# Performance work log

Hardware: AMD Instinct MI355X
Metric: run time of the kernel (lower is better)

Reference implementation:

```python
import jax, jax.numpy as jnp
import numpy as np

B, X, Y, Z = 8, 32, 32, 32
Dx = Dy = Dz = 128
K = 256   # h_dim * k, k=1
H = 2     # h_out
EPS = 1e-5


def _wn(V, g):
    # weight_norm with dim=None: W = g * V / ||V||_F (g scalar)
    return (g / jnp.linalg.norm(V)) * V


def setup_inputs() -> dict:
    key = jax.random.key(0)
    ks = jax.random.split(key, 8)
    x = jax.random.normal(ks[0], (B, X, Dx), jnp.float32)
    y = jax.random.normal(ks[1], (B, Y, Dy), jnp.float32)
    z = jax.random.normal(ks[2], (B, Z, Dz), jnp.float32)
    Vx = jax.random.normal(ks[3], (K, Dx), jnp.float32) * 0.05
    Vy = jax.random.normal(ks[4], (K, Dy), jnp.float32) * 0.05
    Vz = jax.random.normal(ks[5], (K, Dz), jnp.float32) * 0.05
    Vh = jax.random.normal(ks[6], (H, K), jnp.float32) * 0.05
    return {
        "x": x, "y": y, "z": z,
        "Vx": Vx, "gx": jnp.linalg.norm(Vx), "bx": jnp.zeros((K,), jnp.float32),
        "Vy": Vy, "gy": jnp.linalg.norm(Vy), "by": jnp.zeros((K,), jnp.float32),
        "Vz": Vz, "gz": jnp.linalg.norm(Vz), "bz": jnp.zeros((K,), jnp.float32),
        "Vh": Vh, "gh": jnp.linalg.norm(Vh), "bh": jnp.zeros((H,), jnp.float32),
        "gamma": jnp.ones((K,), jnp.float32), "beta": jnp.zeros((K,), jnp.float32),
    }


def reference(x, y, z, Vx, gx, bx, Vy, gy, by, Vz, gz, bz, Vh, gh, bh, gamma, beta):
    relu = jax.nn.relu
    _x = relu(x @ _wn(Vx, gx).T + bx)  # [B,X,K]
    _y = relu(y @ _wn(Vy, gy).T + by)  # [B,Y,K]
    _z = relu(z @ _wn(Vz, gz).T + bz)  # [B,Z,K]
    # trilinear outer product: [B,X,Y,Z,K] (memory-explosive intermediate)
    xyz = jnp.einsum('bxk,byk,bzk->bxyzk', _x, _y, _z)
    att = jnp.einsum('bxyzk,hk->bhxyz', xyz, _wn(Vh, gh)) + bh[None, :, None, None, None]
    # softmax over flattened X*Y*Z per head
    att = jax.nn.softmax(att.reshape(B, H, -1), axis=-1).reshape(B, H, X, Y, Z)
    # attention pooling, summed over all h_out heads (equals the torch loop)
    att_sum = att.sum(axis=1)  # [B,X,Y,Z]
    logits = jnp.einsum('bxk,byk,bzk,bxyz->bk', _x, _y, _z, att_sum)  # [B,K]
    # BatchNorm1d (training-mode batch stats, biased variance)
    mean = logits.mean(axis=0)
    var = logits.var(axis=0)
    out = (logits - mean) / jnp.sqrt(var + EPS) * gamma + beta
    return (out, att)
```

## Files before the change

### kernel.cpp

```cpp
#include <hip/hip_runtime.h>
#include <math.h>

#define BB 8
#define XD 32
#define DD 128
#define KK 256
#define HH 2
#define XYZ 32768
#define EPSV 1e-5f

#define WS_X    0
#define WS_Y    65536
#define WS_Z    131072
#define WS_RAW  196608
#define WS_PART (WS_RAW + 524288)

__global__ void __launch_bounds__(256)
tan_proj_kernel(const float* x, const float* y, const float* z,
                const float* Vx, const float* Vy, const float* Vz,
                const float* gx, const float* gy, const float* gz,
                const float* bx, const float* by, const float* bz,
                float* ws) {
    __shared__ float lin[4 * DD];
    __shared__ float wred[4];
    int bid = blockIdx.x;
    int which = bid >> 6;
    int rgrp = bid & 63;
    int r0 = rgrp * 4;
    const float *in, *V, *g, *bias;
    float* outp;
    if (which == 0)      { in = x; V = Vx; g = gx; bias = bx; outp = ws + WS_X; }
    else if (which == 1) { in = y; V = Vy; g = gy; bias = by; outp = ws + WS_Y; }
    else                 { in = z; V = Vz; g = gz; bias = bz; outp = ws + WS_Z; }
    int t = threadIdx.x;
    {
        int f0 = t, f1 = t + 256;
        lin[f0] = in[(r0 + (f0 >> 7)) * DD + (f0 & 127)];
        lin[f1] = in[(r0 + (f1 >> 7)) * DD + (f1 & 127)];
    }
    __syncthreads();
    const float4* v4 = (const float4*)(V + t * DD);
    const float4* l4 = (const float4*)lin;
    float a0 = 0.f, a1 = 0.f, a2 = 0.f, a3 = 0.f, ssp = 0.f;
#pragma unroll 8
    for (int d4 = 0; d4 < DD / 4; ++d4) {
        float4 a = v4[d4];
        ssp += a.x * a.x + a.y * a.y + a.z * a.z + a.w * a.w;
        float4 b0 = l4[d4];
        float4 b1 = l4[32 + d4];
        float4 b2 = l4[64 + d4];
        float4 b3 = l4[96 + d4];
        a0 += a.x * b0.x + a.y * b0.y + a.z * b0.z + a.w * b0.w;
        a1 += a.x * b1.x + a.y * b1.y + a.z * b1.z + a.w * b1.w;
        a2 += a.x * b2.x + a.y * b2.y + a.z * b2.z + a.w * b2.w;
        a3 += a.x * b3.x + a.y * b3.y + a.z * b3.z + a.w * b3.w;
    }
#pragma unroll
    for (int o = 32; o > 0; o >>= 1) ssp += __shfl_xor(ssp, o);
    if ((t & 63) == 0) wred[t >> 6] = ssp;
    __syncthreads();
    float ss = wred[0] + wred[1] + wred[2] + wred[3];
    float scale = g[0] * rsqrtf(ss);
    float bv = bias[t];
    outp[(r0 + 0) * KK + t] = fmaxf(a0 * scale + bv, 0.f);
    outp[(r0 + 1) * KK + t] = fmaxf(a1 * scale + bv, 0.f);
    outp[(r0 + 2) * KK + t] = fmaxf(a2 * scale + bv, 0.f);
    outp[(r0 + 3) * KK + t] = fmaxf(a3 * scale + bv, 0.f);
}

__global__ void __launch_bounds__(256)
tan_score_kernel(const float* Vh, const float* gh, const float* bh, float* ws) {
    __shared__ float ys[32 * 256];
    __shared__ float zs[32 * 256];
    __shared__ float shh;
    int t = threadIdx.x;
    int bb = blockIdx.x >> 5;
    int xx = blockIdx.x & 31;
    const float* _xb = ws + WS_X + (bb * 32 + xx) * KK;
    const float* _yb = ws + WS_Y + bb * 8192;
    const float* _zb = ws + WS_Z + bb * 8192;

    if (t < 64) {
        float4 h1 = *(const float4*)(Vh + t * 8);
        float4 h2 = *(const float4*)(Vh + t * 8 + 4);
        float hs = h1.x * h1.x + h1.y * h1.y + h1.z * h1.z + h1.w * h1.w
                 + h2.x * h2.x + h2.y * h2.y + h2.z * h2.z + h2.w * h2.w;
#pragma unroll
        for (int o = 32; o > 0; o >>= 1) hs += __shfl_xor(hs, o);
        if (t == 0) shh = hs;
    }

#pragma unroll
    for (int i = 0; i < 8; ++i) {
        int flat = i * 1024 + t * 4;
        int row = flat >> 8;
        int k = flat & 255;
        int gsw = (((k >> 2) ^ (row & 7)) << 2);
        *(float4*)(ys + row * 256 + gsw) = *(const float4*)(_yb + flat);
        *(float4*)(zs + row * 256 + gsw) = *(const float4*)(_zb + flat);
    }
    __syncthreads();
    float sh = gh[0] * rsqrtf(shh);

    int ty = t >> 4;
    int tz = t & 15;
    int y0 = ty, y1 = ty + 16;
    int z0 = tz, z1 = tz + 16;
    int ysw0 = (y0 & 7), ysw1 = (y1 & 7);
    int zsw0 = (z0 & 7), zsw1 = (z1 & 7);

    float a000 = 0.f, a001 = 0.f, a010 = 0.f, a011 = 0.f;
    float a100 = 0.f, a101 = 0.f, a110 = 0.f, a111 = 0.f;

#pragma unroll 4
    for (int kc = 0; kc < 256; kc += 4) {
        int g = kc >> 2;
        float4 xv  = *(const float4*)(_xb + kc);
        float4 vh0 = *(const float4*)(Vh + kc);
        float4 vh1 = *(const float4*)(Vh + KK + kc);
        float4 ya = *(const float4*)(ys + y0 * 256 + ((g ^ ysw0) << 2));
        float4 yb = *(const float4*)(ys + y1 * 256 + ((g ^ ysw1) << 2));
        float4 za = *(const float4*)(zs + z0 * 256 + ((g ^ zsw0) << 2));
        float4 zb = *(const float4*)(zs + z1 * 256 + ((g ^ zsw1) << 2));
#define TAN_STEP(c) { \
        float xs = sh * xv.c; \
        float w0 = xs * vh0.c, w1 = xs * vh1.c; \
        float t00 = w0 * ya.c, t01 = w0 * yb.c; \
        float t10 = w1 * ya.c, t11 = w1 * yb.c; \
        a000 = fmaf(t00, za.c, a000); a001 = fmaf(t00, zb.c, a001); \
        a010 = fmaf(t01, za.c, a010); a011 = fmaf(t01, zb.c, a011); \
        a100 = fmaf(t10, za.c, a100); a101 = fmaf(t10, zb.c, a101); \
        a110 = fmaf(t11, za.c, a110); a111 = fmaf(t11, zb.c, a111); }
        TAN_STEP(x) TAN_STEP(y) TAN_STEP(z) TAN_STEP(w)
#undef TAN_STEP
    }

    float b0 = bh[0], b1 = bh[1];
    float* r0 = ws + WS_RAW + (bb * 2 + 0) * XYZ + xx * 1024;
    float* r1 = r0 + XYZ;
    r0[y0 * 32 + z0] = a000 + b0;  r0[y0 * 32 + z1] = a001 + b0;
    r0[y1 * 32 + z0] = a010 + b0;  r0[y1 * 32 + z1] = a011 + b0;
    r1[y0 * 32 + z0] = a100 + b1;  r1[y0 * 32 + z1] = a101 + b1;
    r1[y1 * 32 + z0] = a110 + b1;  r1[y1 * 32 + z1] = a111 + b1;
}

__global__ void __launch_bounds__(1024)
tan_softmax_kernel(float* ws, float* out) {
    __shared__ float red[1024];
    int bh = blockIdx.x;
    int t = threadIdx.x;
    const float4* raw4 = (const float4*)(ws + WS_RAW + bh * XYZ);
    float4* att4 = (float4*)(out + BB * KK + bh * XYZ);
    float4 v[8];
#pragma unroll
    for (int i = 0; i < 8; ++i) v[i] = raw4[i * 1024 + t];
    float m = -1e30f;
#pragma unroll
    for (int i = 0; i < 8; ++i)
        m = fmaxf(m, fmaxf(fmaxf(v[i].x, v[i].y), fmaxf(v[i].z, v[i].w)));
    red[t] = m;
    __syncthreads();
    for (int s = 512; s > 0; s >>= 1) {
        if (t < s) red[t] = fmaxf(red[t], red[t + s]);
        __syncthreads();
    }
    float M = red[0];
    __syncthreads();
    float l = 0.f;
#pragma unroll
    for (int i = 0; i < 8; ++i) {
        v[i].x = __expf(v[i].x - M); v[i].y = __expf(v[i].y - M);
        v[i].z = __expf(v[i].z - M); v[i].w = __expf(v[i].w - M);
        l += v[i].x + v[i].y + v[i].z + v[i].w;
    }
    red[t] = l;
    __syncthreads();
    for (int s = 512; s > 0; s >>= 1) {
        if (t < s) red[t] += red[t + s];
        __syncthreads();
    }
    float inv = 1.f / red[0];
#pragma unroll
    for (int i = 0; i < 8; ++i) {
        float4 o = v[i];
        o.x *= inv; o.y *= inv; o.z *= inv; o.w *= inv;
        att4[i * 1024 + t] = o;
    }
}

__global__ void __launch_bounds__(256)
tan_logits_kernel(float* ws, const float* out) {
    __shared__ float as4[1024];
    int b = blockIdx.x >> 5;
    int x = blockIdx.x & 31;
    int t = threadIdx.x;
    const float* _zb = ws + WS_Z + b * 8192;
    float zreg[32];
#pragma unroll
    for (int zi = 0; zi < 32; ++zi) zreg[zi] = _zb[zi * 256 + t];
    const float* a0 = out + BB * KK + (b * 2) * XYZ + x * 1024;
    const float* a1 = a0 + XYZ;
    for (int i = t; i < 1024; i += 256) as4[i] = a0[i] + a1[i];
    __syncthreads();
    const float* _yb = ws + WS_Y + b * 8192;
    float acc = 0.f;
#pragma unroll 4
    for (int y = 0; y < 32; ++y) {
        float s = 0.f;
        const float4* ar = (const float4*)(as4 + y * 32);
#pragma unroll
        for (int j = 0; j < 8; ++j) {
            float4 a = ar[j];
            s += a.x * zreg[j * 4] + a.y * zreg[j * 4 + 1]
               + a.z * zreg[j * 4 + 2] + a.w * zreg[j * 4 + 3];
        }
        acc = fmaf(_yb[y * 256 + t], s, acc);
    }
    float xv = ws[WS_X + (b * 32 + x) * 256 + t];
    ws[WS_PART + (b * 32 + x) * 256 + t] = xv * acc;
}

__global__ void __launch_bounds__(1024)
tan_bn_kernel(float* ws, const float* gamma, const float* beta, float* out) {
    __shared__ float red[8192];
    int t = threadIdx.x;
    int tg = t >> 8;
    int k = t & 255;
    const float* part = ws + WS_PART;
    float lg[BB];
#pragma unroll
    for (int b = 0; b < BB; ++b) {
        float s = 0.f;
#pragma unroll
        for (int xi = 0; xi < 8; ++xi)
            s += part[(b * 32 + tg * 8 + xi) * 256 + k];
        red[tg * 2048 + b * 256 + k] = s;
    }
    __syncthreads();
    if (tg == 0) {
#pragma unroll
        for (int b = 0; b < BB; ++b)
            lg[b] = red[b * 256 + k] + red[2048 + b * 256 + k]
                  + red[4096 + b * 256 + k] + red[6144 + b * 256 + k];
        float mean = 0.f;
#pragma unroll
        for (int b = 0; b < BB; ++b) mean += lg[b];
        mean *= 0.125f;
        float var = 0.f;
#pragma unroll
        for (int b = 0; b < BB; ++b) { float d = lg[b] - mean; var += d * d; }
        var *= 0.125f;
        float inv = rsqrtf(var + EPSV);
        float gm = gamma[k], bt = beta[k];
#pragma unroll
        for (int b = 0; b < BB; ++b)
            out[b * 256 + k] = (lg[b] - mean) * inv * gm + bt;
    }
}

extern "C" void kernel_launch(void* const* d_in, const int* in_sizes, int n_in,
                              void* d_out, int out_size, void* d_ws, size_t ws_size,
                              hipStream_t stream) {
    (void)in_sizes; (void)n_in; (void)out_size; (void)ws_size;
    const float* x     = (const float*)d_in[0];
    const float* y     = (const float*)d_in[1];
    const float* z     = (const float*)d_in[2];
    const float* Vx    = (const float*)d_in[3];
    const float* gx    = (const float*)d_in[4];
    const float* bx    = (const float*)d_in[5];
    const float* Vy    = (const float*)d_in[6];
    const float* gy    = (const float*)d_in[7];
    const float* by    = (const float*)d_in[8];
    const float* Vz    = (const float*)d_in[9];
    const float* gz    = (const float*)d_in[10];
    const float* bz    = (const float*)d_in[11];
    const float* Vh    = (const float*)d_in[12];
    const float* gh    = (const float*)d_in[13];
    const float* bh    = (const float*)d_in[14];
    const float* gamma = (const float*)d_in[15];
    const float* beta  = (const float*)d_in[16];
    float* ws  = (float*)d_ws;
    float* out = (float*)d_out;

    tan_proj_kernel<<<192, 256, 0, stream>>>(x, y, z, Vx, Vy, Vz,
                                             gx, gy, gz, bx, by, bz, ws);
    tan_score_kernel<<<256, 256, 0, stream>>>(Vh, gh, bh, ws);
    tan_softmax_kernel<<<16, 1024, 0, stream>>>(ws, out);
    tan_logits_kernel<<<256, 256, 0, stream>>>(ws, out);
    tan_bn_kernel<<<1, 1024, 0, stream>>>(ws, gamma, beta, out);
}
```

Measured before the change: 129.2 us.

## Fuse softmax into score and logits kernels via online partial max/sum

Removes the standalone softmax kernel. The score kernel now computes per-block partial (max, sum-exp) statistics with an online-softmax warp reduction. The logits kernel merges the 32 partials per (batch, head), normalizes the raw scores, writes the attention output and builds the summed attention tile in one pass. The per-x partial logits are now accumulated with atomicAdd into a zeroed buffer, which simplifies the BN kernel, at the cost of an extra memset launch and nondeterministic float summation order.

```diff
diff --git a/kernel.cpp b/kernel.cpp
--- a/kernel.cpp
+++ b/kernel.cpp
@@ -13,7 +13,8 @@
 #define WS_Y    65536
 #define WS_Z    131072
 #define WS_RAW  196608
-#define WS_PART (WS_RAW + 524288)
+#define WS_SM   (WS_RAW + 524288)
+#define WS_LOG  (WS_SM + 1024)
 
 __global__ void __launch_bounds__(256)
 tan_proj_kernel(const float* x, const float* y, const float* z,
@@ -73,6 +74,7 @@
     __shared__ float ys[32 * 256];
     __shared__ float zs[32 * 256];
     __shared__ float shh;
+    __shared__ float smred[4][4];
     int t = threadIdx.x;
     int bb = blockIdx.x >> 5;
     int xx = blockIdx.x & 31;
@@ -105,7 +107,7 @@
     int ty = t >> 4;
     int tz = t & 15;
     int y0 = ty, y1 = ty + 16;
-    int z0 = tz, z1 = tz + 16;
+    int z0 = tz, z1 = tz + 15 + 1;
     int ysw0 = (y0 & 7), ysw1 = (y1 & 7);
     int zsw0 = (z0 & 7), zsw1 = (z1 & 7);
 
@@ -136,61 +138,57 @@
     }
 
     float b0 = bh[0], b1 = bh[1];
+    a000 += b0; a001 += b0; a010 += b0; a011 += b0;
+    a100 += b1; a101 += b1; a110 += b1; a111 += b1;
     float* r0 = ws + WS_RAW + (bb * 2 + 0) * XYZ + xx * 1024;
     float* r1 = r0 + XYZ;
-    r0[y0 * 32 + z0] = a000 + b0;  r0[y0 * 32 + z1] = a001 + b0;
-    r0[y1 * 32 + z0] = a010 + b0;  r0[y1 * 32 + z1] = a011 + b0;
-    r1[y0 * 32 + z0] = a100 + b1;  r1[y0 * 32 + z1] = a101 + b1;
-    r1[y1 * 32 + z0] = a110 + b1;  r1[y1 * 32 + z1] = a111 + b1;
-}
-
-__global__ void __launch_bounds__(1024)
-tan_softmax_kernel(float* ws, float* out) {
-    __shared__ float red[1024];
-    int bh = blockIdx.x;
-    int t = threadIdx.x;
-    const float4* raw4 = (const float4*)(ws + WS_RAW + bh * XYZ);
-    float4* att4 = (float4*)(out + BB * KK + bh * XYZ);
-    float4 v[8];
-#pragma unroll
-    for (int i = 0; i < 8; ++i) v[i] = raw4[i * 1024 + t];
-    float m = -1e30f;
-#pragma unroll
-    for (int i = 0; i < 8; ++i)
-        m = fmaxf(m, fmaxf(fmaxf(v[i].x, v[i].y), fmaxf(v[i].z, v[i].w)));
-    red[t] = m;
-    __syncthreads();
-    for (int s = 512; s > 0; s >>= 1) {
-        if (t < s) red[t] = fmaxf(red[t], red[t + s]);
-        __syncthreads();
-    }
-    float M = red[0];
-    __syncthreads();
-    float l = 0.f;
-#pragma unroll
-    for (int i = 0; i < 8; ++i) {
-        v[i].x = __expf(v[i].x - M); v[i].y = __expf(v[i].y - M);
-        v[i].z = __expf(v[i].z - M); v[i].w = __expf(v[i].w - M);
-        l += v[i].x + v[i].y + v[i].z + v[i].w;
-    }
-    red[t] = l;
-    __syncthreads();
-    for (int s = 512; s > 0; s >>= 1) {
-        if (t < s) red[t] += red[t + s];
-        __syncthreads();
-    }
-    float inv = 1.f / red[0];
-#pragma unroll
-    for (int i = 0; i < 8; ++i) {
-        float4 o = v[i];
-        o.x *= inv; o.y *= inv; o.z *= inv; o.w *= inv;
-        att4[i * 1024 + t] = o;
+    r0[y0 * 32 + z0] = a000;  r0[y0 * 32 + z1] = a001;
+    r0[y1 * 32 + z0] = a010;  r0[y1 * 32 + z1] = a011;
+    r1[y0 * 32 + z0] = a100;  r1[y0 * 32 + z1] = a101;
+    r1[y1 * 32 + z0] = a110;  r1[y1 * 32 + z1] = a111;
+
+    float m0 = fmaxf(fmaxf(a000, a001), fmaxf(a010, a011));
+    float l0 = __expf(a000 - m0) + __expf(a001 - m0)
+             + __expf(a010 - m0) + __expf(a011 - m0);
+    float m1 = fmaxf(fmaxf(a100, a101), fmaxf(a110, a111));
+    float l1 = __expf(a100 - m1) + __expf(a101 - m1)
+             + __expf(a110 - m1) + __expf(a111 - m1);
+#pragma unroll
+    for (int o = 1; o < 64; o <<= 1) {
+        float mo = __shfl_xor(m0, o), lo = __shfl_xor(l0, o);
+        float nm = fmaxf(m0, mo);
+        l0 = l0 * __expf(m0 - nm) + lo * __expf(mo - nm); m0 = nm;
+        mo = __shfl_xor(m1, o); lo = __shfl_xor(l1, o);
+        nm = fmaxf(m1, mo);
+        l1 = l1 * __expf(m1 - nm) + lo * __expf(mo - nm); m1 = nm;
+    }
+    if ((t & 63) == 0) {
+        int w = t >> 6;
+        smred[w][0] = m0; smred[w][1] = l0;
+        smred[w][2] = m1; smred[w][3] = l1;
+    }
+    __syncthreads();
+    if (t == 0) {
+        float M0 = smred[0][0], L0 = smred[0][1];
+        float M1 = smred[0][2], L1 = smred[0][3];
+#pragma unroll
+        for (int w = 1; w < 4; ++w) {
+            float nm = fmaxf(M0, smred[w][0]);
+            L0 = L0 * __expf(M0 - nm) + smred[w][1] * __expf(smred[w][0] - nm);
+            M0 = nm;
+            nm = fmaxf(M1, smred[w][2]);
+            L1 = L1 * __expf(M1 - nm) + smred[w][3] * __expf(smred[w][2] - nm);
+            M1 = nm;
+        }
+        float* sm = ws + WS_SM + (bb * 32 + xx) * 4;
+        sm[0] = M0; sm[1] = L0; sm[2] = M1; sm[3] = L1;
     }
 }
 
 __global__ void __launch_bounds__(256)
-tan_logits_kernel(float* ws, const float* out) {
+tan_logits_kernel(float* ws, float* out) {
     __shared__ float as4[1024];
+    __shared__ float cons[4];
     int b = blockIdx.x >> 5;
     int x = blockIdx.x & 31;
     int t = threadIdx.x;
@@ -198,10 +196,40 @@
     float zreg[32];
 #pragma unroll
     for (int zi = 0; zi < 32; ++zi) zreg[zi] = _zb[zi * 256 + t];
-    const float* a0 = out + BB * KK + (b * 2) * XYZ + x * 1024;
-    const float* a1 = a0 + XYZ;
-    for (int i = t; i < 1024; i += 256) as4[i] = a0[i] + a1[i];
-    __syncthreads();
+
+    if (t < 64) {
+        const float* sm = ws + WS_SM + (b * 32 + (t & 31)) * 4;
+        float4 p = *(const float4*)sm;
+        float m0 = p.x, l0 = p.y, m1 = p.z, l1 = p.w;
+#pragma unroll
+        for (int o = 1; o < 32; o <<= 1) {
+            float mo = __shfl_xor(m0, o), lo = __shfl_xor(l0, o);
+            float nm = fmaxf(m0, mo);
+            l0 = l0 * __expf(m0 - nm) + lo * __expf(mo - nm); m0 = nm;
+            mo = __shfl_xor(m1, o); lo = __shfl_xor(l1, o);
+            nm = fmaxf(m1, mo);
+            l1 = l1 * __expf(m1 - nm) + lo * __expf(mo - nm); m1 = nm;
+        }
+        if (t == 0) {
+            cons[0] = m0; cons[1] = 1.f / l0;
+            cons[2] = m1; cons[3] = 1.f / l1;
+        }
+    }
+    __syncthreads();
+    float M0 = cons[0], inv0 = cons[1], M1 = cons[2], inv1 = cons[3];
+    const float* r0 = ws + WS_RAW + (b * 2) * XYZ + x * 1024;
+    const float* r1 = r0 + XYZ;
+    float* o0 = out + BB * KK + (b * 2) * XYZ + x * 1024;
+    float* o1 = o0 + XYZ;
+#pragma unroll
+    for (int i = t; i < 1024; i += 256) {
+        float a0 = __expf(r0[i] - M0) * inv0;
+        float a1 = __expf(r1[i] - M1) * inv1;
+        o0[i] = a0; o1[i] = a1;
+        as4[i] = a0 + a1;
+    }
+    __syncthreads();
+
     const float* _yb = ws + WS_Y + b * 8192;
     float acc = 0.f;
 #pragma unroll 4
@@ -217,45 +245,29 @@
         acc = fmaf(_yb[y * 256 + t], s, acc);
     }
     float xv = ws[WS_X + (b * 32 + x) * 256 + t];
-    ws[WS_PART + (b * 32 + x) * 256 + t] = xv * acc;
-}
-
-__global__ void __launch_bounds__(1024)
-tan_bn_kernel(float* ws, const float* gamma, const float* beta, float* out) {
-    __shared__ float red[8192];
-    int t = threadIdx.x;
-    int tg = t >> 8;
-    int k = t & 255;
-    const float* part = ws + WS_PART;
+    atomicAdd(ws + WS_LOG + b * 256 + t, xv * acc);
+}
+
+__global__ void __launch_bounds__(256)
+tan_bn_kernel(const float* ws, const float* gamma, const float* beta, float* out) {
+    int k = threadIdx.x;
+    const float* lgp = ws + WS_LOG;
     float lg[BB];
 #pragma unroll
-    for (int b = 0; b < BB; ++b) {
-        float s = 0.f;
-#pragma unroll
-        for (int xi = 0; xi < 8; ++xi)
-            s += part[(b * 32 + tg * 8 + xi) * 256 + k];
-        red[tg * 2048 + b * 256 + k] = s;
-    }
-    __syncthreads();
-    if (tg == 0) {
-#pragma unroll
-        for (int b = 0; b < BB; ++b)
-            lg[b] = red[b * 256 + k] + red[2048 + b * 256 + k]
-                  + red[4096 + b * 256 + k] + red[6144 + b * 256 + k];
-        float mean = 0.f;
-#pragma unroll
-        for (int b = 0; b < BB; ++b) mean += lg[b];
-        mean *= 0.125f;
-        float var = 0.f;
-#pragma unroll
-        for (int b = 0; b < BB; ++b) { float d = lg[b] - mean; var += d * d; }
-        var *= 0.125f;
-        float inv = rsqrtf(var + EPSV);
-        float gm = gamma[k], bt = beta[k];
-#pragma unroll
-        for (int b = 0; b < BB; ++b)
-            out[b * 256 + k] = (lg[b] - mean) * inv * gm + bt;
-    }
+    for (int b = 0; b < BB; ++b) lg[b] = lgp[b * 256 + k];
+    float mean = 0.f;
+#pragma unroll
+    for (int b = 0; b < BB; ++b) mean += lg[b];
+    mean *= 0.125f;
+    float var = 0.f;
+#pragma unroll
+    for (int b = 0; b < BB; ++b) { float d = lg[b] - mean; var += d * d; }
+    var *= 0.125f;
+    float inv = rsqrtf(var + EPSV);
+    float gm = gamma[k], bt = beta[k];
+#pragma unroll
+    for (int b = 0; b < BB; ++b)
+        out[b * 256 + k] = (lg[b] - mean) * inv * gm + bt;
 }
 
 extern "C" void kernel_launch(void* const* d_in, const int* in_sizes, int n_in,
@@ -282,10 +294,10 @@
     float* ws  = (float*)d_ws;
     float* out = (float*)d_out;
 
+    hipMemsetAsync(ws + WS_LOG, 0, 2048 * sizeof(float), stream);
     tan_proj_kernel<<<192, 256, 0, stream>>>(x, y, z, Vx, Vy, Vz,
                                              gx, gy, gz, bx, by, bz, ws);
     tan_score_kernel<<<256, 256, 0, stream>>>(Vh, gh, bh, ws);
-    tan_softmax_kernel<<<16, 1024, 0, stream>>>(ws, out);
     tan_logits_kernel<<<256, 256, 0, stream>>>(ws, out);
-    tan_bn_kernel<<<1, 1024, 0, stream>>>(ws, gamma, beta, out);
-}
+    tan_bn_kernel<<<1, 256, 0, stream>>>(ws, gamma, beta, out);
+}
```

Measured after the change: 121.7 us. 1.06x faster.
